# Kernel optimization log

Hardware: AMD Instinct MI355X
Metric: run time of the kernel (lower is better)

Reference implementation:

```python
import jax, jax.numpy as jnp
import numpy as np

N_NODES = 50000
IN_F = 128
OUT_F = 128
N_EDGES = 800000
ALPHA = 0.2  # LeakyReLU negative slope
EPS = 1e-16

def _xavier(key, shape, gain=1.414):
    fan_in, fan_out = shape[0], shape[1]
    bound = gain * np.sqrt(6.0 / (fan_in + fan_out))
    return jax.random.uniform(key, shape, jnp.float32, -bound, bound)

def setup_inputs() -> dict:
    key = jax.random.key(0)
    k_h, k_e, k_W, k_a = jax.random.split(key, 4)
    h = jax.random.normal(k_h, (N_NODES, IN_F), dtype=jnp.float32)
    edge_index = jax.random.randint(k_e, (2, N_EDGES), 0, N_NODES, dtype=jnp.int64)
    W = _xavier(k_W, (IN_F, OUT_F))
    a = _xavier(k_a, (2 * OUT_F, 1))
    return {"h": h, "edge_index": edge_index, "W": W, "a": a}

def reference(h, edge_index, W, a):
    # h: [N, F_in], edge_index: [2, E], W: [F_in, F_out], a: [2*F_out, 1]
    Wh = h @ W                                   # [N, F_out]
    row, col = edge_index[0], edge_index[1]
    # cat([Wh_i, Wh_j]) @ a  ==  Wh_i @ a1 + Wh_j @ a2  (compute per-node, gather per-edge)
    a1, a2 = a[:OUT_F, 0], a[OUT_F:, 0]
    s1 = Wh @ a1                                 # [N]
    s2 = Wh @ a2                                 # [N]
    e = jax.nn.leaky_relu(s1[row] + s2[col], negative_slope=ALPHA)  # [E]
    # NOTE: original code's "e_rowmax" is actually a segment SUM (index_add_), replicated faithfully
    e_rowsum = jax.ops.segment_sum(e, row, num_segments=N_NODES)    # [N]
    e_exp = jnp.exp(e - e_rowsum[row])                              # [E]
    e_exp_sum = jax.ops.segment_sum(e_exp, row, num_segments=N_NODES)
    attention = e_exp / (e_exp_sum[row] + EPS)                      # [E]
    # weighted scatter-add aggregation
    h_prime = jax.ops.segment_sum(attention[:, None] * Wh[col], row, num_segments=N_NODES)
    return h_prime
```

## Files before the change

### kernel.cpp

```cpp
#include <hip/hip_runtime.h>
#include <hip/hip_bf16.h>
#include <math.h>

#define NNODES 50000
#define NF 128
#define NEDGES 800000
#define ALPHA 0.2f
#define EPS 1e-16f
#define GEMM_BLOCKS 782
#define NCHUNK 128
#define ECHUNK 6250
#define NHW 12500
#define CAP 64

typedef __attribute__((ext_vector_type(8))) short bf16x8;
typedef __attribute__((ext_vector_type(4))) float f32x4;

__device__ inline unsigned bf16rne(float x) {
    unsigned u = __float_as_uint(x);
    return (u + 0x7FFFu + ((u >> 16) & 1u)) >> 16;
}
__device__ inline float bflo(unsigned u) { return __uint_as_float(u << 16); }
__device__ inline float bfhi(unsigned u) { return __uint_as_float(u & 0xFFFF0000u); }

__global__ __launch_bounds__(256) void prep(const float* __restrict__ W,
                                            const float* __restrict__ a,
                                            ushort* __restrict__ WbF,
                                            float* __restrict__ Wa1,
                                            float* __restrict__ Wa2) {
    if (blockIdx.x < 8) {
        int s = blockIdx.x * 256 + threadIdx.x;
        int l = s & 63;
        int ct = (s >> 6) & 7;
        int ks = s >> 9;
        int c = ct * 16 + (l & 15);
        int g = l >> 4;
        ushort v[8];
        #pragma unroll
        for (int j = 0; j < 8; ++j) {
            int k = ks * 32 + ((j >> 2) << 4) + g * 4 + (j & 3);
            v[j] = (ushort)bf16rne(W[k * NF + c]);
        }
        *(uint4*)&WbF[(size_t)s * 8] = *(uint4*)v;
    } else {
        int k = threadIdx.x;
        if (k < NF) {
            float t1 = 0.f, t2 = 0.f;
            for (int c = 0; c < NF; ++c) {
                float w = W[k * NF + c];
                t1 += w * a[c];
                t2 += w * a[NF + c];
            }
            Wa1[k] = t1;
            Wa2[k] = t2;
        }
    }
}

__global__ __launch_bounds__(256) void gemm_hist(const float* __restrict__ h,
                                                 const ushort* __restrict__ WbF,
                                                 const float* __restrict__ Wa1,
                                                 const float* __restrict__ Wa2,
                                                 const int* __restrict__ ei,
                                                 ushort* __restrict__ WhBu,
                                                 float* __restrict__ s1,
                                                 float* __restrict__ s2,
                                                 unsigned char* __restrict__ H) {
    __shared__ char lds[NHW * 4];
    const int tid = threadIdx.x;

    if (blockIdx.x < NCHUNK) {
        unsigned* hist = (unsigned*)lds;
        for (int i = tid; i < NHW; i += 256) hist[i] = 0u;
        __syncthreads();
        const int e0 = blockIdx.x * ECHUNK;
        for (int i = tid; i < ECHUNK; i += 256) {
            int r = ei[e0 + i];
            atomicAdd(&hist[r >> 2], 1u << (8 * (r & 3)));
        }
        __syncthreads();
        unsigned* Hc = (unsigned*)&H[(size_t)blockIdx.x * NNODES];
        for (int i = tid; i < NHW; i += 256) Hc[i] = hist[i];
        return;
    }

    const int bid = blockIdx.x - NCHUNK;
    ushort* ldsB = (ushort*)lds;

    #pragma unroll
    for (int i = 0; i < 8; ++i) {
        int off8 = (tid + i * 256) * 8;
        *(uint4*)&ldsB[off8] = *(const uint4*)&WbF[off8];
    }
    __syncthreads();

    const int lane = tid & 63;
    const int wrow = tid >> 6;
    const int m = lane & 15;
    const int g = lane >> 4;
    const int row = bid * 64 + wrow * 16 + m;
    const int rowc = (row < NNODES) ? row : 0;

    f32x4 acc[8];
    #pragma unroll
    for (int t = 0; t < 8; ++t) acc[t] = (f32x4){0.f, 0.f, 0.f, 0.f};

    float p1 = 0.f, p2 = 0.f;
    #pragma unroll
    for (int ks = 0; ks < 4; ++ks) {
        const float4 ha = *(const float4*)&h[(size_t)rowc * NF + ks * 32 + g * 4];
        const float4 hb = *(const float4*)&h[(size_t)rowc * NF + ks * 32 + 16 + g * 4];
        const float4 wa1a = *(const float4*)&Wa1[ks * 32 + g * 4];
        const float4 wa1b = *(const float4*)&Wa1[ks * 32 + 16 + g * 4];
        const float4 wa2a = *(const float4*)&Wa2[ks * 32 + g * 4];
        const float4 wa2b = *(const float4*)&Wa2[ks * 32 + 16 + g * 4];
        p1 += ha.x * wa1a.x + ha.y * wa1a.y + ha.z * wa1a.z + ha.w * wa1a.w
            + hb.x * wa1b.x + hb.y * wa1b.y + hb.z * wa1b.z + hb.w * wa1b.w;
        p2 += ha.x * wa2a.x + ha.y * wa2a.y + ha.z * wa2a.z + ha.w * wa2a.w
            + hb.x * wa2b.x + hb.y * wa2b.y + hb.z * wa2b.z + hb.w * wa2b.w;
        bf16x8 afrag;
        afrag[0] = (short)bf16rne(ha.x);
        afrag[1] = (short)bf16rne(ha.y);
        afrag[2] = (short)bf16rne(ha.z);
        afrag[3] = (short)bf16rne(ha.w);
        afrag[4] = (short)bf16rne(hb.x);
        afrag[5] = (short)bf16rne(hb.y);
        afrag[6] = (short)bf16rne(hb.z);
        afrag[7] = (short)bf16rne(hb.w);
        #pragma unroll
        for (int ct = 0; ct < 8; ++ct) {
            bf16x8 bfrag = *(bf16x8*)&ldsB[((ks * 8 + ct) * 64 + lane) * 8];
            acc[ct] = __builtin_amdgcn_mfma_f32_16x16x32_bf16(afrag, bfrag, acc[ct], 0, 0, 0);
        }
    }

    p1 += __shfl_xor(p1, 16); p1 += __shfl_xor(p1, 32);
    p2 += __shfl_xor(p2, 16); p2 += __shfl_xor(p2, 32);
    if (g == 0 && row < NNODES) { s1[row] = p1; s2[row] = p2; }

    const int orow = bid * 64 + wrow * 16 + g * 4;
    #pragma unroll
    for (int r = 0; r < 4; ++r) {
        int gr = orow + r;
        if (gr < NNODES) {
            #pragma unroll
            for (int ct = 0; ct < 8; ++ct)
                WhBu[(size_t)gr * NF + ct * 16 + m] = (ushort)bf16rne(acc[ct][r]);
        }
    }
}

__global__ __launch_bounds__(256) void scan_chunks(const unsigned char* __restrict__ H,
                                                   unsigned char* __restrict__ B,
                                                   int* __restrict__ count) {
    const int gid = blockIdx.x * 256 + threadIdx.x;
    const int r0 = gid * 4;
    if (r0 >= NNODES) return;
    unsigned run = 0u;
    for (int c = 0; c < NCHUNK; ++c) {
        unsigned hv = *(const unsigned*)&H[(size_t)c * NNODES + r0];
        *(unsigned*)&B[(size_t)c * NNODES + r0] = run;
        run += hv;
    }
    count[r0 + 0] = run & 0xFF;
    count[r0 + 1] = (run >> 8) & 0xFF;
    count[r0 + 2] = (run >> 16) & 0xFF;
    count[r0 + 3] = (run >> 24) & 0xFF;
}

__global__ __launch_bounds__(256) void scatter(const int* __restrict__ ei,
                                               const unsigned char* __restrict__ B,
                                               ushort* __restrict__ bucket) {
    __shared__ unsigned hist[NHW];
    const int tid = threadIdx.x;
    for (int i = tid; i < NHW; i += 256) hist[i] = 0u;
    __syncthreads();
    const int e0 = blockIdx.x * ECHUNK;
    const unsigned char* Bc = &B[(size_t)blockIdx.x * NNODES];
    for (int i = tid; i < ECHUNK; i += 256) {
        int r = ei[e0 + i];
        int col = ei[NEDGES + e0 + i];
        unsigned old = atomicAdd(&hist[r >> 2], 1u << (8 * (r & 3)));
        int lrank = (old >> (8 * (r & 3))) & 0xFF;
        int pos = (int)Bc[r] + lrank;
        if (pos < CAP)
            bucket[r * CAP + pos] = (ushort)col;
    }
}

__global__ __launch_bounds__(256) void aggregate(const int* __restrict__ count,
                                                 const ushort* __restrict__ colbucket,
                                                 const float* __restrict__ s1,
                                                 const float* __restrict__ s2,
                                                 const unsigned* __restrict__ WhB,
                                                 float* __restrict__ out) {
    const int wid = threadIdx.x >> 6;
    const int lane = threadIdx.x & 63;
    const int row = blockIdx.x * 4 + wid;
    if (row >= NNODES) return;
    const int deg = min(count[row], CAP);

    int cv = 0;
    float ev = 0.f;
    if (lane < deg) cv = (int)colbucket[row * CAP + lane];
    const float s1r = s1[row];
    if (lane < deg) {
        float s = s1r + s2[cv];
        ev = (s >= 0.f) ? s : ALPHA * s;
    }

    float rs = ev;
    #pragma unroll
    for (int off = 32; off; off >>= 1) rs += __shfl_xor(rs, off);
    float xv = (lane < deg) ? expf(ev - rs) : 0.f;
    float ds = xv;
    #pragma unroll
    for (int off = 32; off; off >>= 1) ds += __shfl_xor(ds, off);
    const float invd = 1.0f / (ds + EPS);

    float accx = 0.f, accy = 0.f;
    int j = 0;
    for (; j + 8 <= deg; j += 8) {
        int cc[8]; unsigned u[8]; float ww[8];
        #pragma unroll
        for (int k = 0; k < 8; ++k) cc[k] = __shfl(cv, j + k);
        #pragma unroll
        for (int k = 0; k < 8; ++k) u[k] = WhB[(size_t)cc[k] * 64 + lane];
        #pragma unroll
        for (int k = 0; k < 8; ++k) ww[k] = __shfl(xv, j + k);
        #pragma unroll
        for (int k = 0; k < 8; ++k) {
            float w = ww[k] * invd;
            accx += w * bflo(u[k]);
            accy += w * bfhi(u[k]);
        }
    }
    for (; j < deg; ++j) {
        int c = __shfl(cv, j);
        unsigned u = WhB[(size_t)c * 64 + lane];
        float w = __shfl(xv, j) * invd;
        accx += w * bflo(u);
        accy += w * bfhi(u);
    }
    ((float2*)out)[(size_t)row * 64 + lane] = make_float2(accx, accy);
}

extern "C" void kernel_launch(void* const* d_in, const int* in_sizes, int n_in,
                              void* d_out, int out_size, void* d_ws, size_t ws_size,
                              hipStream_t stream) {
    const float* h  = (const float*)d_in[0];
    const int*   ei = (const int*)d_in[1];
    const float* W  = (const float*)d_in[2];
    const float* a  = (const float*)d_in[3];
    float* out = (float*)d_out;

    char* ws = (char*)d_ws;
    size_t off = 0;
    auto alloc = [&](size_t bytes) -> void* {
        void* p = ws + off;
        off += (bytes + 255) & ~(size_t)255;
        return p;
    };

    unsigned*      WhB    = (unsigned*)alloc((size_t)NNODES * 64 * 4);
    ushort*        bucket = (ushort*)alloc((size_t)NNODES * CAP * 2);
    unsigned char* H      = (unsigned char*)alloc((size_t)NCHUNK * NNODES);
    unsigned char* B      = (unsigned char*)alloc((size_t)NCHUNK * NNODES);
    ushort*        WbF    = (ushort*)alloc((size_t)2048 * 16);
    float*         Wa1    = (float*)alloc((size_t)NF * 4);
    float*         Wa2    = (float*)alloc((size_t)NF * 4);
    int*           count  = (int*)alloc((size_t)NNODES * 4);
    float*         s1     = (float*)alloc((size_t)NNODES * 4);
    float*         s2     = (float*)alloc((size_t)NNODES * 4);

    prep<<<9, 256, 0, stream>>>(W, a, WbF, Wa1, Wa2);
    gemm_hist<<<NCHUNK + GEMM_BLOCKS, 256, 0, stream>>>(
        h, WbF, Wa1, Wa2, ei, (ushort*)WhB, s1, s2, H);
    scan_chunks<<<49, 256, 0, stream>>>(H, B, count);
    scatter<<<NCHUNK, 256, 0, stream>>>(ei, B, bucket);
    aggregate<<<(NNODES + 3) / 4, 256, 0, stream>>>(count, bucket, s1, s2, WhB, out);
}
```

Before: 99.10 us.

## Split GEMM across hist and scan launches, store local ranks for wide scatter

The GEMM work is now split into two halves. One half runs beside the histogram blocks and the other beside the scan blocks, so the latency-bound scan overlaps with useful compute. The histogram pass writes each edge's local rank to a new byte array. This lets scatter drop its LDS histogram rebuild and run as a wide, fully parallel kernel over 782 blocks instead of 128. The trade-off is an extra 800KB write and read of rank bytes, plus a second launch that carries GEMM blocks.

```diff
diff --git a/kernel.cpp b/kernel.cpp
--- a/kernel.cpp
+++ b/kernel.cpp
@@ -7,11 +7,13 @@
 #define NEDGES 800000
 #define ALPHA 0.2f
 #define EPS 1e-16f
-#define GEMM_BLOCKS 782
 #define NCHUNK 128
 #define ECHUNK 6250
 #define NHW 12500
 #define CAP 64
+#define GEMM_A 391
+#define GEMM_B 391
+#define SCAN_BLOCKS 49
 
 typedef __attribute__((ext_vector_type(8))) short bf16x8;
 typedef __attribute__((ext_vector_type(4))) float f32x4;
@@ -57,36 +59,14 @@
     }
 }
 
-__global__ __launch_bounds__(256) void gemm_hist(const float* __restrict__ h,
-                                                 const ushort* __restrict__ WbF,
-                                                 const float* __restrict__ Wa1,
-                                                 const float* __restrict__ Wa2,
-                                                 const int* __restrict__ ei,
-                                                 ushort* __restrict__ WhBu,
-                                                 float* __restrict__ s1,
-                                                 float* __restrict__ s2,
-                                                 unsigned char* __restrict__ H) {
-    __shared__ char lds[NHW * 4];
-    const int tid = threadIdx.x;
-
-    if (blockIdx.x < NCHUNK) {
-        unsigned* hist = (unsigned*)lds;
-        for (int i = tid; i < NHW; i += 256) hist[i] = 0u;
-        __syncthreads();
-        const int e0 = blockIdx.x * ECHUNK;
-        for (int i = tid; i < ECHUNK; i += 256) {
-            int r = ei[e0 + i];
-            atomicAdd(&hist[r >> 2], 1u << (8 * (r & 3)));
-        }
-        __syncthreads();
-        unsigned* Hc = (unsigned*)&H[(size_t)blockIdx.x * NNODES];
-        for (int i = tid; i < NHW; i += 256) Hc[i] = hist[i];
-        return;
-    }
-
-    const int bid = blockIdx.x - NCHUNK;
-    ushort* ldsB = (ushort*)lds;
-
+__device__ __forceinline__ void gemm_body(int bid, ushort* ldsB, int tid,
+                                          const float* __restrict__ h,
+                                          const ushort* __restrict__ WbF,
+                                          const float* __restrict__ Wa1,
+                                          const float* __restrict__ Wa2,
+                                          ushort* __restrict__ WhBu,
+                                          float* __restrict__ s1,
+                                          float* __restrict__ s2) {
     #pragma unroll
     for (int i = 0; i < 8; ++i) {
         int off8 = (tid + i * 256) * 8;
@@ -150,42 +130,97 @@
     }
 }
 
-__global__ __launch_bounds__(256) void scan_chunks(const unsigned char* __restrict__ H,
-                                                   unsigned char* __restrict__ B,
-                                                   int* __restrict__ count) {
-    const int gid = blockIdx.x * 256 + threadIdx.x;
-    const int r0 = gid * 4;
-    if (r0 >= NNODES) return;
-    unsigned run = 0u;
-    for (int c = 0; c < NCHUNK; ++c) {
-        unsigned hv = *(const unsigned*)&H[(size_t)c * NNODES + r0];
-        *(unsigned*)&B[(size_t)c * NNODES + r0] = run;
-        run += hv;
-    }
-    count[r0 + 0] = run & 0xFF;
-    count[r0 + 1] = (run >> 8) & 0xFF;
-    count[r0 + 2] = (run >> 16) & 0xFF;
-    count[r0 + 3] = (run >> 24) & 0xFF;
+__global__ __launch_bounds__(256) void hist_gemm(const float* __restrict__ h,
+                                                 const ushort* __restrict__ WbF,
+                                                 const float* __restrict__ Wa1,
+                                                 const float* __restrict__ Wa2,
+                                                 const int* __restrict__ ei,
+                                                 ushort* __restrict__ WhBu,
+                                                 float* __restrict__ s1,
+                                                 float* __restrict__ s2,
+                                                 unsigned char* __restrict__ H,
+                                                 unsigned char* __restrict__ lrank) {
+    __shared__ char lds[NHW * 4];
+    const int tid = threadIdx.x;
+
+    if (blockIdx.x < NCHUNK) {
+        unsigned* hist = (unsigned*)lds;
+        for (int i = tid; i < NHW; i += 256) hist[i] = 0u;
+        __syncthreads();
+        const int e0 = blockIdx.x * ECHUNK;
+        for (int i = tid; i < ECHUNK; i += 256) {
+            int r = ei[e0 + i];
+            unsigned old = atomicAdd(&hist[r >> 2], 1u << (8 * (r & 3)));
+            lrank[e0 + i] = (unsigned char)((old >> (8 * (r & 3))) & 0xFF);
+        }
+        __syncthreads();
+        unsigned* Hc = (unsigned*)&H[(size_t)blockIdx.x * NNODES];
+        for (int i = tid; i < NHW; i += 256) Hc[i] = hist[i];
+        return;
+    }
+
+    gemm_body(blockIdx.x - NCHUNK, (ushort*)lds, tid, h, WbF, Wa1, Wa2, WhBu, s1, s2);
+}
+
+__global__ __launch_bounds__(256) void scan_gemm(const float* __restrict__ h,
+                                                 const ushort* __restrict__ WbF,
+                                                 const float* __restrict__ Wa1,
+                                                 const float* __restrict__ Wa2,
+                                                 const unsigned char* __restrict__ H,
+                                                 unsigned char* __restrict__ B,
+                                                 int* __restrict__ count,
+                                                 ushort* __restrict__ WhBu,
+                                                 float* __restrict__ s1,
+                                                 float* __restrict__ s2) {
+    __shared__ ushort ldsB[16384];
+    const int tid = threadIdx.x;
+
+    if (blockIdx.x < SCAN_BLOCKS) {
+        const int gid = blockIdx.x * 256 + tid;
+        const int r0 = gid * 4;
+        if (r0 >= NNODES) return;
+        unsigned run = 0u;
+        for (int c = 0; c < NCHUNK; ++c) {
+            unsigned hv = *(const unsigned*)&H[(size_t)c * NNODES + r0];
+            *(unsigned*)&B[(size_t)c * NNODES + r0] = run;
+            run += hv;
+        }
+        count[r0 + 0] = run & 0xFF;
+        count[r0 + 1] = (run >> 8) & 0xFF;
+        count[r0 + 2] = (run >> 16) & 0xFF;
+        count[r0 + 3] = (run >> 24) & 0xFF;
+        return;
+    }
+
+    gemm_body(GEMM_A + (blockIdx.x - SCAN_BLOCKS), ldsB, tid, h, WbF, Wa1, Wa2, WhBu, s1, s2);
 }
 
 __global__ __launch_bounds__(256) void scatter(const int* __restrict__ ei,
+                                               const unsigned char* __restrict__ lrank,
                                                const unsigned char* __restrict__ B,
                                                ushort* __restrict__ bucket) {
-    __shared__ unsigned hist[NHW];
-    const int tid = threadIdx.x;
-    for (int i = tid; i < NHW; i += 256) hist[i] = 0u;
-    __syncthreads();
-    const int e0 = blockIdx.x * ECHUNK;
-    const unsigned char* Bc = &B[(size_t)blockIdx.x * NNODES];
-    for (int i = tid; i < ECHUNK; i += 256) {
-        int r = ei[e0 + i];
-        int col = ei[NEDGES + e0 + i];
-        unsigned old = atomicAdd(&hist[r >> 2], 1u << (8 * (r & 3)));
-        int lrank = (old >> (8 * (r & 3))) & 0xFF;
-        int pos = (int)Bc[r] + lrank;
-        if (pos < CAP)
-            bucket[r * CAP + pos] = (ushort)col;
-    }
+    const int base = blockIdx.x * 1024 + threadIdx.x;
+    int idx[4], r[4], c[4], lr[4];
+    #pragma unroll
+    for (int k = 0; k < 4; ++k) {
+        idx[k] = base + k * 256;
+        if (idx[k] < NEDGES) {
+            r[k] = ei[idx[k]];
+            c[k] = ei[NEDGES + idx[k]];
+            lr[k] = (int)lrank[idx[k]];
+        } else r[k] = -1;
+    }
+    int pos[4];
+    #pragma unroll
+    for (int k = 0; k < 4; ++k)
+        if (r[k] >= 0) {
+            int ch = idx[k] / ECHUNK;
+            pos[k] = (int)B[(size_t)ch * NNODES + r[k]] + lr[k];
+        }
+    #pragma unroll
+    for (int k = 0; k < 4; ++k)
+        if (r[k] >= 0 && pos[k] < CAP)
+            bucket[r[k] * CAP + pos[k]] = (ushort)c[k];
 }
 
 __global__ __launch_bounds__(256) void aggregate(const int* __restrict__ count,
@@ -266,6 +301,7 @@
     ushort*        bucket = (ushort*)alloc((size_t)NNODES * CAP * 2);
     unsigned char* H      = (unsigned char*)alloc((size_t)NCHUNK * NNODES);
     unsigned char* B      = (unsigned char*)alloc((size_t)NCHUNK * NNODES);
+    unsigned char* lrank  = (unsigned char*)alloc((size_t)NEDGES);
     ushort*        WbF    = (ushort*)alloc((size_t)2048 * 16);
     float*         Wa1    = (float*)alloc((size_t)NF * 4);
     float*         Wa2    = (float*)alloc((size_t)NF * 4);
@@ -274,9 +310,10 @@
     float*         s2     = (float*)alloc((size_t)NNODES * 4);
 
     prep<<<9, 256, 0, stream>>>(W, a, WbF, Wa1, Wa2);
-    gemm_hist<<<NCHUNK + GEMM_BLOCKS, 256, 0, stream>>>(
-        h, WbF, Wa1, Wa2, ei, (ushort*)WhB, s1, s2, H);
-    scan_chunks<<<49, 256, 0, stream>>>(H, B, count);
-    scatter<<<NCHUNK, 256, 0, stream>>>(ei, B, bucket);
+    hist_gemm<<<NCHUNK + GEMM_A, 256, 0, stream>>>(
+        h, WbF, Wa1, Wa2, ei, (ushort*)WhB, s1, s2, H, lrank);
+    scan_gemm<<<SCAN_BLOCKS + GEMM_B, 256, 0, stream>>>(
+        h, WbF, Wa1, Wa2, H, B, count, (ushort*)WhB, s1, s2);
+    scatter<<<(NEDGES + 1023) / 1024, 256, 0, stream>>>(ei, lrank, B, bucket);
     aggregate<<<(NNODES + 3) / 4, 256, 0, stream>>>(count, bucket, s1, s2, WhB, out);
 }
```

After: 84.68 us (median of 2 runs). -14.6%, faster.
